# Optimization experiments

Measured on AMD Instinct MI355X. Metric: run time of the kernel, lower is better.

Reference implementation:

```python
import jax, jax.numpy as jnp
import numpy as np

EPS = 1e-5
NH, KD, D = 16, 16, 64  # num_heads, key_dim, per-head value dim (attn_ratio*key_dim)


def _bn(x, g, b):
    # train-mode BatchNorm1d over [B, C, N]: stats over (B, N), biased variance
    m = jnp.mean(x, axis=(0, 2), keepdims=True)
    v = jnp.var(x, axis=(0, 2), keepdims=True)
    return (x - m) * jax.lax.rsqrt(v + EPS) * g[None, :, None] + b[None, :, None]


def _relu6(x):
    return jnp.clip(x, 0.0, 6.0)


def setup_inputs() -> dict:
    key = jax.random.key(0)
    ks = jax.random.split(key, 8)
    B, C, H, W = 8, 256, 32, 32
    dim, dh, hid = 256, NH * D, 1024

    def w(k, shape):
        return jax.random.normal(k, shape, dtype=jnp.float32) * 0.02

    return {
        "x": jax.random.normal(ks[0], (B, C, H, W), dtype=jnp.float32),
        "g1": jnp.ones((dim,), jnp.float32), "b1": jnp.zeros((dim,), jnp.float32),
        "wq": w(ks[1], (NH * KD, dim)), "bq": jnp.zeros((NH * KD,), jnp.float32),
        "wk": w(ks[2], (NH * KD, dim)), "bk": jnp.zeros((NH * KD,), jnp.float32),
        "wv": w(ks[3], (dh, dim)), "bv": jnp.zeros((dh,), jnp.float32),
        "wp": w(ks[4], (dim, dh)), "bp": jnp.zeros((dim,), jnp.float32),
        "g2": jnp.ones((dim,), jnp.float32), "b2": jnp.zeros((dim,), jnp.float32),
        "w1": w(ks[5], (hid, dim)), "bb1": jnp.zeros((hid,), jnp.float32),
        "w2": w(ks[6], (dim, hid)), "bb2": jnp.zeros((dim,), jnp.float32),
    }


def reference(x, g1, b1, wq, bq, wk, bk, wv, bv, wp, bp, g2, b2, w1, bb1, w2, bb2):
    B, C, H, W = x.shape
    N = H * W
    xf = x.reshape(B, C, N)

    # --- attention branch (dropout is identity in eval/reference) ---
    y = _bn(xf, g1, b1)
    q = (jnp.einsum('bcn,oc->bon', y, wq) + bq[None, :, None]).reshape(B, NH, KD, N).transpose(0, 1, 3, 2)  # [B,h,N,kd]
    k = jnp.einsum('bcn,oc->bon', y, wk) + bk[None, :, None]
    k = k.reshape(B, NH, KD, N)                                                                           # [B,h,kd,N]
    v = (jnp.einsum('bcn,oc->bon', y, wv) + bv[None, :, None]).reshape(B, NH, D, N).transpose(0, 1, 3, 2)  # [B,h,N,d]
    # torch code divides by scale = key_dim**-0.5, i.e. multiplies by sqrt(key_dim)
    attn = jax.nn.softmax(jnp.einsum('bhnk,bhkm->bhnm', q, k) / (KD ** -0.5), axis=-1)
    o = jnp.einsum('bhnm,bhmd->bhnd', attn, v).transpose(0, 1, 3, 2).reshape(B, NH * D, N)                 # [B,dh,N]
    o = jnp.einsum('bdn,od->bon', o, wp) + bp[None, :, None]                                               # [B,C,N]
    xf = xf + o

    # --- MLP branch: Linear(dim->hid) + ReLU6 + Conv1d(hid->dim, k=1) ---
    y2 = _bn(xf, g2, b2)
    h = _relu6(jnp.einsum('bcn,hc->bhn', y2, w1) + bb1[None, :, None])
    m = jnp.einsum('bhn,oh->bon', h, w2) + bb2[None, :, None]
    xf = xf + m

    return xf.reshape(B, C, H, W)
```

## Files before the change

### kernel.cpp

```cpp
#include <hip/hip_runtime.h>
#include <hip/hip_bf16.h>
#include <cstdint>


typedef __attribute__((ext_vector_type(8))) short short8;
typedef __attribute__((ext_vector_type(4))) float floatx4;

#define QK_SC 5.770780163555851f

__device__ __forceinline__ float b2f(unsigned short u) {
  union { unsigned int i; float f; } x; x.i = ((unsigned int)u) << 16; return x.f;
}
__device__ __forceinline__ unsigned short f2b(float f) {
  union { float f; unsigned int i; } x; x.f = f;
  unsigned int r = x.i + 0x7FFFu + ((x.i >> 16) & 1u);
  return (unsigned short)(r >> 16);
}
__device__ __forceinline__ unsigned int f2b2(float a, float b) {
  __hip_bfloat162 h = __float22bfloat162_rn(make_float2(a, b));
  union { __hip_bfloat162 v; unsigned int u; } x; x.v = h; return x.u;
}

__global__ __launch_bounds__(256) void prep(
    const float* __restrict__ s0, const float* __restrict__ s1,
    const float* __restrict__ s2, const float* __restrict__ s3,
    const float* __restrict__ s4, const float* __restrict__ s5,
    unsigned short* __restrict__ dst,
    const float* __restrict__ x, float* __restrict__ acc,
    const float* __restrict__ bq, const float* __restrict__ bk,
    const float* __restrict__ bv, float* __restrict__ biasqkv) {
  int blk = blockIdx.x, t = threadIdx.x;
  if (blk < 1152) {
    int i = blk * 256 + t;
    if (i >= 294912) return;
    const float* s; int li; size_t dbase;
    if (i < 16384)       { s = s0; li = i;          dbase = 0; }
    else if (i < 32768)  { s = s1; li = i - 16384;  dbase = 65536; }
    else if (i < 98304)  { s = s2; li = i - 32768;  dbase = 131072; }
    else if (i < 163840) { s = s3; li = i - 98304;  dbase = 393216; }
    else if (i < 229376) { s = s4; li = i - 163840; dbase = 655360; }
    else                 { s = s5; li = i - 229376; dbase = 917504; }
    float4 v = ((const float4*)s)[li];
    uint2 o; o.x = f2b2(v.x, v.y); o.y = f2b2(v.z, v.w);
    ((uint2*)(dst + dbase))[li] = o;
  } else if (blk < 3200) {
    int blk2 = blk - 1152;
    int b = blk2 >> 8, c = blk2 & 255;
    const float* p = x + (((size_t)(b * 256 + c)) << 10);
    float4 v = ((const float4*)p)[t];
    float s = (v.x + v.y) + (v.z + v.w);
    float s2 = (v.x * v.x + v.y * v.y) + (v.z * v.z + v.w * v.w);
    #pragma unroll
    for (int o = 32; o > 0; o >>= 1) { s += __shfl_down(s, o, 64); s2 += __shfl_down(s2, o, 64); }
    __shared__ float rs[4], rs2[4];
    int w = t >> 6;
    if ((t & 63) == 0) { rs[w] = s; rs2[w] = s2; }
    __syncthreads();
    if (t == 0) {
      atomicAdd(acc + c, (rs[0] + rs[1]) + (rs[2] + rs[3]));
      atomicAdd(acc + 256 + c, (rs2[0] + rs2[1]) + (rs2[2] + rs2[3]));
    }
  } else {
    int i = (blk - 3200) * 256 + t;
    float v = (i < 256) ? bq[i] : (i < 512) ? bk[i - 256] : bv[i - 512];
    biasqkv[i] = v;
  }
}

__global__ __launch_bounds__(256) void bn_apply_t(
    const float* __restrict__ x, const float* __restrict__ acc,
    const float* __restrict__ g, const float* __restrict__ bb,
    unsigned short* __restrict__ yt) {
  int nt = blockIdx.x, ct = blockIdx.y, b = blockIdx.z;
  int t = threadIdx.x;
  __shared__ unsigned short T[64][72];
  {
    int r = t >> 2, g4 = (t & 3) * 16;
    int c = ct * 64 + r;
    float m = acc[c] * (1.0f / 8192.0f);
    float var = acc[256 + c] * (1.0f / 8192.0f) - m * m;
    float scl = g[c] * rsqrtf(var + 1e-5f);
    float shf = bb[c] - m * scl;
    const float* p = x + (((size_t)(b * 256 + c)) << 10) + nt * 64 + g4;
    float4 u0 = *(const float4*)(p);
    float4 u1 = *(const float4*)(p + 4);
    float4 u2 = *(const float4*)(p + 8);
    float4 u3 = *(const float4*)(p + 12);
    uint4 o0, o1;
    o0.x = f2b2(fmaf(u0.x, scl, shf), fmaf(u0.y, scl, shf));
    o0.y = f2b2(fmaf(u0.z, scl, shf), fmaf(u0.w, scl, shf));
    o0.z = f2b2(fmaf(u1.x, scl, shf), fmaf(u1.y, scl, shf));
    o0.w = f2b2(fmaf(u1.z, scl, shf), fmaf(u1.w, scl, shf));
    o1.x = f2b2(fmaf(u2.x, scl, shf), fmaf(u2.y, scl, shf));
    o1.y = f2b2(fmaf(u2.z, scl, shf), fmaf(u2.w, scl, shf));
    o1.z = f2b2(fmaf(u3.x, scl, shf), fmaf(u3.y, scl, shf));
    o1.w = f2b2(fmaf(u3.z, scl, shf), fmaf(u3.w, scl, shf));
    *(uint4*)&T[r][g4] = o0;
    *(uint4*)&T[r][g4 + 8] = o1;
  }
  __syncthreads();
  {
    int nr = t >> 2, cg = (t & 3) * 16;
    unsigned int ob[8];
    #pragma unroll
    for (int j = 0; j < 8; ++j) {
      unsigned int lo = T[cg + 2 * j][nr];
      unsigned int hi = T[cg + 2 * j + 1][nr];
      ob[j] = lo | (hi << 16);
    }
    unsigned short* orow = yt + ((size_t)(b * 1024 + nt * 64 + nr)) * 256 + ct * 64 + cg;
    *(uint4*)&orow[0] = make_uint4(ob[0], ob[1], ob[2], ob[3]);
    *(uint4*)&orow[8] = make_uint4(ob[4], ob[5], ob[6], ob[7]);
  }
}

template <int MODE>
__global__ __launch_bounds__(256, 4) void gemm3(
    const unsigned short* __restrict__ W, const unsigned short* __restrict__ Bn,
    const float* __restrict__ bias, const float* __restrict__ resf,
    const unsigned short* __restrict__ resb, void* __restrict__ outv,
    float* __restrict__ stats, const float* __restrict__ bnin,
    const float* __restrict__ g, const float* __restrict__ bb, int M, int K) {
  int bid = blockIdx.x;
  int b = bid & 7;
  int rest = bid >> 3;
  int n0 = (rest & 15) * 64, m0 = (rest >> 4) * 64;
  int t = threadIdx.x, lane = t & 63, w = t >> 6;
  int ml = lane & 15, quad = lane >> 4;

  __shared__ unsigned short Wt[64][72];
  __shared__ unsigned short Yt[64][72];
  __shared__ float Scl[256], Shf[256];

  if (MODE == 6) {
    float m = bnin[t] * (1.0f / 8192.0f);
    float var = bnin[256 + t] * (1.0f / 8192.0f) - m * m;
    float scl = g[t] * rsqrtf(var + 1e-5f);
    Scl[t] = scl;
    Shf[t] = bb[t] - m * scl;
    __syncthreads();
  }

  const unsigned short* Bp = Bn + (size_t)b * 1024 * K;
  int sr = t >> 2, scg = (t & 3) * 16;
  const unsigned short* wrow = W + (size_t)(m0 + sr) * K + scg;
  const unsigned short* brow = Bp + (size_t)(n0 + sr) * K + scg;

  floatx4 acc[4];
  #pragma unroll
  for (int i = 0; i < 4; ++i) acc[i] = (floatx4){0.f, 0.f, 0.f, 0.f};

  for (int k0 = 0; k0 < K; k0 += 64) {
    *(uint4*)&Wt[sr][scg]     = *(const uint4*)(wrow + k0);
    *(uint4*)&Wt[sr][scg + 8] = *(const uint4*)(wrow + k0 + 8);
    if (MODE == 6) {
      uint4 r0 = *(const uint4*)(brow + k0);
      uint4 r1 = *(const uint4*)(brow + k0 + 8);
      int cb = k0 + scg;
      float4 s0 = *(const float4*)&Scl[cb],     h0 = *(const float4*)&Shf[cb];
      float4 s1 = *(const float4*)&Scl[cb + 4], h1 = *(const float4*)&Shf[cb + 4];
      float4 s2 = *(const float4*)&Scl[cb + 8], h2 = *(const float4*)&Shf[cb + 8];
      float4 s3 = *(const float4*)&Scl[cb + 12], h3 = *(const float4*)&Shf[cb + 12];
      uint4 o0, o1;
      o0.x = f2b2(fmaf(b2f(r0.x & 0xffff), s0.x, h0.x), fmaf(b2f(r0.x >> 16), s0.y, h0.y));
      o0.y = f2b2(fmaf(b2f(r0.y & 0xffff), s0.z, h0.z), fmaf(b2f(r0.y >> 16), s0.w, h0.w));
      o0.z = f2b2(fmaf(b2f(r0.z & 0xffff), s1.x, h1.x), fmaf(b2f(r0.z >> 16), s1.y, h1.y));
      o0.w = f2b2(fmaf(b2f(r0.w & 0xffff), s1.z, h1.z), fmaf(b2f(r0.w >> 16), s1.w, h1.w));
      o1.x = f2b2(fmaf(b2f(r1.x & 0xffff), s2.x, h2.x), fmaf(b2f(r1.x >> 16), s2.y, h2.y));
      o1.y = f2b2(fmaf(b2f(r1.y & 0xffff), s2.z, h2.z), fmaf(b2f(r1.y >> 16), s2.w, h2.w));
      o1.z = f2b2(fmaf(b2f(r1.z & 0xffff), s3.x, h3.x), fmaf(b2f(r1.z >> 16), s3.y, h3.y));
      o1.w = f2b2(fmaf(b2f(r1.w & 0xffff), s3.z, h3.z), fmaf(b2f(r1.w >> 16), s3.w, h3.w));
      *(uint4*)&Yt[sr][scg]     = o0;
      *(uint4*)&Yt[sr][scg + 8] = o1;
    } else {
      *(uint4*)&Yt[sr][scg]     = *(const uint4*)(brow + k0);
      *(uint4*)&Yt[sr][scg + 8] = *(const uint4*)(brow + k0 + 8);
    }
    __syncthreads();
    short8 a0 = *(const short8*)&Wt[w * 16 + ml][quad * 8];
    short8 a1 = *(const short8*)&Wt[w * 16 + ml][32 + quad * 8];
    #pragma unroll
    for (int nt2 = 0; nt2 < 4; ++nt2) {
      short8 b0 = *(const short8*)&Yt[nt2 * 16 + ml][quad * 8];
      short8 b1 = *(const short8*)&Yt[nt2 * 16 + ml][32 + quad * 8];
      acc[nt2] = __builtin_amdgcn_mfma_f32_16x16x32_bf16(a0, b0, acc[nt2], 0, 0, 0);
      acc[nt2] = __builtin_amdgcn_mfma_f32_16x16x32_bf16(a1, b1, acc[nt2], 0, 0, 0);
    }
    __syncthreads();
  }

  int row_base = m0 + w * 16 + quad * 4;

  if (MODE == 4) {
    int hh = row_base >> 4;
    float b0 = bias[row_base + 0], b1 = bias[row_base + 1];
    float b2 = bias[row_base + 2], b3 = bias[row_base + 3];
    if (hh < 32) {
      unsigned short* qkout = (unsigned short*)outv + ((hh < 16) ? 0 : 2097152);
      float os = (hh < 16) ? QK_SC : 1.0f;
      int head = hh & 15, kd0 = row_base & 15;
      #pragma unroll
      for (int c = 0; c < 4; ++c) {
        int col = n0 + c * 16 + ml;
        uint2 pw;
        pw.x = f2b2((acc[c][0] + b0) * os, (acc[c][1] + b1) * os);
        pw.y = f2b2((acc[c][2] + b2) * os, (acc[c][3] + b3) * os);
        *(uint2*)&qkout[(((size_t)b * 16 + head) * 1024 + col) * 16 + kd0] = pw;
      }
    } else {
      unsigned short* vout = (unsigned short*)outv + 4194304;
      int d0 = row_base - 512;
      #pragma unroll
      for (int c = 0; c < 4; ++c) {
        int col = n0 + c * 16 + ml;
        vout[((size_t)b * 1024 + d0 + 0) * 1024 + col] = f2b(acc[c][0] + b0);
        vout[((size_t)b * 1024 + d0 + 1) * 1024 + col] = f2b(acc[c][1] + b1);
        vout[((size_t)b * 1024 + d0 + 2) * 1024 + col] = f2b(acc[c][2] + b2);
        vout[((size_t)b * 1024 + d0 + 3) * 1024 + col] = f2b(acc[c][3] + b3);
      }
    }
  } else if (MODE == 5) {
    unsigned short* outp = (unsigned short*)outv;
    float vsum[4] = {0.f, 0.f, 0.f, 0.f}, vsq[4] = {0.f, 0.f, 0.f, 0.f};
    #pragma unroll
    for (int c = 0; c < 4; ++c) {
      int col = n0 + c * 16 + ml;
      float v0 = acc[c][0] + bias[row_base + 0] + resf[((size_t)b * 256 + row_base + 0) * 1024 + col];
      float v1 = acc[c][1] + bias[row_base + 1] + resf[((size_t)b * 256 + row_base + 1) * 1024 + col];
      float v2 = acc[c][2] + bias[row_base + 2] + resf[((size_t)b * 256 + row_base + 2) * 1024 + col];
      float v3 = acc[c][3] + bias[row_base + 3] + resf[((size_t)b * 256 + row_base + 3) * 1024 + col];
      vsum[0] += v0; vsq[0] += v0 * v0;
      vsum[1] += v1; vsq[1] += v1 * v1;
      vsum[2] += v2; vsq[2] += v2 * v2;
      vsum[3] += v3; vsq[3] += v3 * v3;
      uint2 pw; pw.x = f2b2(v0, v1); pw.y = f2b2(v2, v3);
      *(uint2*)&outp[((size_t)b * 1024 + col) * 256 + row_base] = pw;
    }
    #pragma unroll
    for (int r = 0; r < 4; ++r) {
      float s = vsum[r], q = vsq[r];
      #pragma unroll
      for (int o = 1; o < 16; o <<= 1) { s += __shfl_xor(s, o, 64); q += __shfl_xor(q, o, 64); }
      if (ml == 0) {
        atomicAdd(stats + row_base + r, s);
        atomicAdd(stats + 256 + row_base + r, q);
      }
    }
  } else if (MODE == 6) {
    unsigned short* outp = (unsigned short*)outv;
    #pragma unroll
    for (int c = 0; c < 4; ++c) {
      int col = n0 + c * 16 + ml;
      float v0 = fminf(fmaxf(acc[c][0] + bias[row_base + 0], 0.f), 6.f);
      float v1 = fminf(fmaxf(acc[c][1] + bias[row_base + 1], 0.f), 6.f);
      float v2 = fminf(fmaxf(acc[c][2] + bias[row_base + 2], 0.f), 6.f);
      float v3 = fminf(fmaxf(acc[c][3] + bias[row_base + 3], 0.f), 6.f);
      uint2 pw; pw.x = f2b2(v0, v1); pw.y = f2b2(v2, v3);
      *(uint2*)&outp[((size_t)b * 1024 + col) * 1024 + row_base] = pw;
    }
  } else {
    float* outp = (float*)outv;
    #pragma unroll
    for (int c = 0; c < 4; ++c) {
      int col = n0 + c * 16 + ml;
      uint2 rv = *(const uint2*)(resb + ((size_t)b * 1024 + col) * 256 + row_base);
      float r0 = b2f((unsigned short)(rv.x & 0xffff));
      float r1 = b2f((unsigned short)(rv.x >> 16));
      float r2 = b2f((unsigned short)(rv.y & 0xffff));
      float r3 = b2f((unsigned short)(rv.y >> 16));
      outp[((size_t)b * 256 + row_base + 0) * 1024 + col] = acc[c][0] + bias[row_base + 0] + r0;
      outp[((size_t)b * 256 + row_base + 1) * 1024 + col] = acc[c][1] + bias[row_base + 1] + r1;
      outp[((size_t)b * 256 + row_base + 2) * 1024 + col] = acc[c][2] + bias[row_base + 2] + r2;
      outp[((size_t)b * 256 + row_base + 3) * 1024 + col] = acc[c][3] + bias[row_base + 3] + r3;
    }
  }
}

__global__ __launch_bounds__(256, 4) void attn_kernel(
    const unsigned short* __restrict__ qt, const unsigned short* __restrict__ kt,
    const unsigned short* __restrict__ vt, unsigned short* __restrict__ ot) {
  int bx0 = blockIdx.x;
  int bx = (bx0 & 7) * 128 + (bx0 >> 3);
  int nt = bx & 7, h = (bx >> 3) & 15, b = bx >> 7;
  int tid = threadIdx.x, lane = tid & 63, w = tid >> 6;
  int ml = lane & 15, quad = lane >> 4;

  __shared__ unsigned int Pscr[4][2][2][16][18];
  __shared__ float Ssum[4][2][16];

  const int n0 = nt * 128 + w * 32;
  const size_t qk_row = ((size_t)b * 16 + h) * 1024;

  short8 qf[2];
  #pragma unroll
  for (int rg = 0; rg < 2; ++rg) {
    short8 z = {0, 0, 0, 0, 0, 0, 0, 0};
    if (quad < 2)
      z = *(const short8*)(qt + (qk_row + n0 + rg * 16 + ml) * 16 + quad * 8);
    qf[rg] = z;
  }

  const floatx4 zf = {0.f, 0.f, 0.f, 0.f};
  floatx4 oacc[2][4];
  #pragma unroll
  for (int rg = 0; rg < 2; ++rg)
    #pragma unroll
    for (int dt = 0; dt < 4; ++dt) oacc[rg][dt] = zf;
  float psum0 = 0.f, psum1 = 0.f;

  const unsigned short* kp = kt + qk_row * 16;
  const unsigned short* vp = vt + ((size_t)b * 1024 + h * 64) * 1024;

  #pragma unroll 2
  for (int mc = 0; mc < 1024; mc += 32) {
    int buf = (mc >> 5) & 1;
    short8 kf[2];
    #pragma unroll
    for (int tt = 0; tt < 2; ++tt) {
      short8 z = {0, 0, 0, 0, 0, 0, 0, 0};
      if (quad < 2)
        z = *(const short8*)(kp + (size_t)(mc + tt * 16 + ml) * 16 + quad * 8);
      kf[tt] = z;
    }
    short8 vf[4];
    #pragma unroll
    for (int dt = 0; dt < 4; ++dt)
      vf[dt] = *(const short8*)(vp + (size_t)(dt * 16 + ml) * 1024 + mc + quad * 8);

    #pragma unroll
    for (int rg = 0; rg < 2; ++rg) {
      #pragma unroll
      for (int tt = 0; tt < 2; ++tt) {
        floatx4 s = __builtin_amdgcn_mfma_f32_16x16x32_bf16(kf[tt], qf[rg], zf, 0, 0, 0);
        float p0 = __builtin_amdgcn_exp2f(s[0]);
        float p1 = __builtin_amdgcn_exp2f(s[1]);
        float p2 = __builtin_amdgcn_exp2f(s[2]);
        float p3 = __builtin_amdgcn_exp2f(s[3]);
        if (rg == 0) psum0 += (p0 + p1) + (p2 + p3);
        else         psum1 += (p0 + p1) + (p2 + p3);
        uint2 pw; pw.x = f2b2(p0, p1); pw.y = f2b2(p2, p3);
        *(uint2*)&Pscr[w][buf][rg][ml][tt * 8 + quad * 2] = pw;
      }
    }
    #pragma unroll
    for (int rg = 0; rg < 2; ++rg) {
      uint2 a0 = *(const uint2*)&Pscr[w][buf][rg][ml][quad * 4];
      uint2 a1 = *(const uint2*)&Pscr[w][buf][rg][ml][quad * 4 + 2];
      union { uint4 u; short8 s; } cv;
      cv.u = make_uint4(a0.x, a0.y, a1.x, a1.y);
      short8 af = cv.s;
      #pragma unroll
      for (int dt = 0; dt < 4; ++dt)
        oacc[rg][dt] = __builtin_amdgcn_mfma_f32_16x16x32_bf16(af, vf[dt], oacc[rg][dt], 0, 0, 0);
    }
  }

  {
    float s0 = psum0;
    s0 += __shfl_xor(s0, 16, 64);
    s0 += __shfl_xor(s0, 32, 64);
    float s1 = psum1;
    s1 += __shfl_xor(s1, 16, 64);
    s1 += __shfl_xor(s1, 32, 64);
    if (lane < 16) { Ssum[w][0][ml] = s0; Ssum[w][1][ml] = s1; }
  }
  #pragma unroll
  for (int rg = 0; rg < 2; ++rg) {
    float4 sv = *(const float4*)&Ssum[w][rg][quad * 4];
    float inv0 = 1.0f / sv.x, inv1 = 1.0f / sv.y;
    float inv2 = 1.0f / sv.z, inv3 = 1.0f / sv.w;
    int nbase = n0 + rg * 16 + quad * 4;
    #pragma unroll
    for (int dt = 0; dt < 4; ++dt) {
      int dg = h * 64 + dt * 16 + ml;
      size_t obase = (((size_t)b << 10) + nbase) * 1024 + dg;
      ot[obase + 0 * 1024] = f2b(oacc[rg][dt][0] * inv0);
      ot[obase + 1 * 1024] = f2b(oacc[rg][dt][1] * inv1);
      ot[obase + 2 * 1024] = f2b(oacc[rg][dt][2] * inv2);
      ot[obase + 3 * 1024] = f2b(oacc[rg][dt][3] * inv3);
    }
  }
}

extern "C" void kernel_launch(void* const* d_in, const int* in_sizes, int n_in,
                              void* d_out, int out_size, void* d_ws, size_t ws_size,
                              hipStream_t stream) {
  const float* x   = (const float*)d_in[0];
  const float* g1  = (const float*)d_in[1];
  const float* b1  = (const float*)d_in[2];
  const float* wq  = (const float*)d_in[3];
  const float* bq  = (const float*)d_in[4];
  const float* wk  = (const float*)d_in[5];
  const float* bk  = (const float*)d_in[6];
  const float* wv  = (const float*)d_in[7];
  const float* bv  = (const float*)d_in[8];
  const float* wp  = (const float*)d_in[9];
  const float* bp  = (const float*)d_in[10];
  const float* g2  = (const float*)d_in[11];
  const float* b2  = (const float*)d_in[12];
  const float* w1  = (const float*)d_in[13];
  const float* bb1 = (const float*)d_in[14];
  const float* w2  = (const float*)d_in[15];
  const float* bb2 = (const float*)d_in[16];

  char* ws = (char*)d_ws;
  float* bnacc   = (float*)ws;
  float* biasqkv = (float*)(ws + 4096);
  unsigned short* y_t  = (unsigned short*)(ws + 16384);
  unsigned short* qt   = y_t + (size_t)2 * 1024 * 1024;
  unsigned short* kt   = qt  + (size_t)2 * 1024 * 1024;
  unsigned short* vt   = kt  + (size_t)2 * 1024 * 1024;
  unsigned short* ot   = vt  + (size_t)8 * 1024 * 1024;
  unsigned short* xf1t = ot  + (size_t)8 * 1024 * 1024;
  unsigned short* wb   = xf1t + (size_t)2 * 1024 * 1024;
  unsigned short* hb_t = ot;
  float* outp = (float*)d_out;

  unsigned short* wqkvb = wb;
  unsigned short* wpb = wb + 393216;
  unsigned short* w1b = wb + 655360;
  unsigned short* w2b = wb + 917504;
  const unsigned short* nub = nullptr;
  const float* nuf = nullptr;

  hipMemsetAsync(bnacc, 0, 4096, stream);
  prep<<<dim3(3206), dim3(256), 0, stream>>>(
      wq, wk, wv, wp, w1, w2, wb, x, bnacc, bq, bk, bv, biasqkv);

  bn_apply_t<<<dim3(16, 4, 8), dim3(256), 0, stream>>>(x, bnacc, g1, b1, y_t);
  gemm3<4><<<dim3(3072), dim3(256), 0, stream>>>(
      wqkvb, y_t, biasqkv, nuf, nub, qt, nullptr, nuf, nuf, nuf, 1536, 256);
  attn_kernel<<<dim3(1024), dim3(256), 0, stream>>>(qt, kt, vt, ot);
  gemm3<5><<<dim3(512), dim3(256), 0, stream>>>(
      wpb, ot, bp, x, nub, xf1t, bnacc + 512, nuf, nuf, nuf, 256, 1024);

  gemm3<6><<<dim3(2048), dim3(256), 0, stream>>>(
      w1b, xf1t, bb1, nuf, nub, hb_t, nullptr, bnacc + 512, g2, b2, 1024, 256);
  gemm3<7><<<dim3(512), dim3(256), 0, stream>>>(
      w2b, hb_t, bb2, nuf, xf1t, outp, nullptr, nuf, nuf, nuf, 256, 1024);
}
```

Baseline: 245.0 us.

## Software-pipeline attention loop: prefetch next K/V tiles and overlap QK with PV

Restructures the attention inner loop into a two-stage software pipeline. K and V for upcoming tiles are loaded into double-buffered registers, and the QK^T/exp step for the next tile is interleaved with the PV MFMA for the previous tile. The goal is to hide global-load latency and the LDS round-trip of P behind matrix work. In exchange it raises register pressure, which could reduce occupancy.

```diff
diff --git a/kernel.cpp b/kernel.cpp
--- a/kernel.cpp
+++ b/kernel.cpp
@@ -311,22 +311,23 @@
   const unsigned short* kp = kt + qk_row * 16;
   const unsigned short* vp = vt + ((size_t)b * 1024 + h * 64) * 1024;
 
-  #pragma unroll 2
-  for (int mc = 0; mc < 1024; mc += 32) {
-    int buf = (mc >> 5) & 1;
-    short8 kf[2];
+  auto loadK = [&](int tile, short8* dst) {
+    int mc = tile << 5;
     #pragma unroll
     for (int tt = 0; tt < 2; ++tt) {
       short8 z = {0, 0, 0, 0, 0, 0, 0, 0};
       if (quad < 2)
         z = *(const short8*)(kp + (size_t)(mc + tt * 16 + ml) * 16 + quad * 8);
-      kf[tt] = z;
-    }
-    short8 vf[4];
+      dst[tt] = z;
+    }
+  };
+  auto loadV = [&](int tile, short8* dst) {
+    int mc = tile << 5;
     #pragma unroll
     for (int dt = 0; dt < 4; ++dt)
-      vf[dt] = *(const short8*)(vp + (size_t)(dt * 16 + ml) * 1024 + mc + quad * 8);
-
+      dst[dt] = *(const short8*)(vp + (size_t)(dt * 16 + ml) * 1024 + mc + quad * 8);
+  };
+  auto qkstep = [&](const short8* kf, int bufidx) {
     #pragma unroll
     for (int rg = 0; rg < 2; ++rg) {
       #pragma unroll
@@ -339,20 +340,56 @@
         if (rg == 0) psum0 += (p0 + p1) + (p2 + p3);
         else         psum1 += (p0 + p1) + (p2 + p3);
         uint2 pw; pw.x = f2b2(p0, p1); pw.y = f2b2(p2, p3);
-        *(uint2*)&Pscr[w][buf][rg][ml][tt * 8 + quad * 2] = pw;
+        *(uint2*)&Pscr[w][bufidx][rg][ml][tt * 8 + quad * 2] = pw;
       }
     }
+  };
+  auto readP = [&](int bufidx, short8* af) {
     #pragma unroll
     for (int rg = 0; rg < 2; ++rg) {
-      uint2 a0 = *(const uint2*)&Pscr[w][buf][rg][ml][quad * 4];
-      uint2 a1 = *(const uint2*)&Pscr[w][buf][rg][ml][quad * 4 + 2];
+      uint2 a0 = *(const uint2*)&Pscr[w][bufidx][rg][ml][quad * 4];
+      uint2 a1 = *(const uint2*)&Pscr[w][bufidx][rg][ml][quad * 4 + 2];
       union { uint4 u; short8 s; } cv;
       cv.u = make_uint4(a0.x, a0.y, a1.x, a1.y);
-      short8 af = cv.s;
+      af[rg] = cv.s;
+    }
+  };
+  auto pvstep = [&](const short8* af, const short8* vf) {
+    #pragma unroll
+    for (int rg = 0; rg < 2; ++rg)
       #pragma unroll
       for (int dt = 0; dt < 4; ++dt)
-        oacc[rg][dt] = __builtin_amdgcn_mfma_f32_16x16x32_bf16(af, vf[dt], oacc[rg][dt], 0, 0, 0);
-    }
+        oacc[rg][dt] = __builtin_amdgcn_mfma_f32_16x16x32_bf16(af[rg], vf[dt], oacc[rg][dt], 0, 0, 0);
+  };
+
+  short8 kfA[2], kfB[2], vfA[4], vfB[4];
+
+  loadK(0, kfA); loadV(0, vfA);
+  qkstep(kfA, 0);
+  loadK(1, kfB); loadV(1, vfB);
+
+  for (int j = 0; j < 15; ++j) {
+    int i = 2 * j + 1;
+    short8 pa[2];
+    readP(0, pa);
+    loadK(i + 1, kfA);
+    qkstep(kfB, 1);
+    pvstep(pa, vfA);
+    loadV(i + 1, vfA);
+    readP(1, pa);
+    loadK(i + 2, kfB);
+    qkstep(kfA, 0);
+    pvstep(pa, vfB);
+    loadV(i + 2, vfB);
+  }
+
+  {
+    short8 pa[2];
+    readP(0, pa);
+    qkstep(kfB, 1);
+    pvstep(pa, vfA);
+    readP(1, pa);
+    pvstep(pa, vfB);
   }
 
   {
```

New measurement: 268.2 us. +9.5%, slower.

## Split attention key range across two wave groups with LDS reduction

Applied to the files above, without the earlier changes.

Doubles the attention block to 512 threads. Each of the two 4-wave halves processes half of the 1024 keys for the same 128 queries, and the partial outputs and row sums are combined through shared memory before normalization. The softmax has no max subtraction, so the two partials can simply be added. This halves the serial loop length per wave and raises wave-level parallelism, at the cost of extra LDS traffic, two block barriers and higher per-block register/LDS pressure.

```diff
diff --git a/kernel.cpp b/kernel.cpp
--- a/kernel.cpp
+++ b/kernel.cpp
@@ -276,19 +276,20 @@
   }
 }
 
-__global__ __launch_bounds__(256, 4) void attn_kernel(
+__global__ __launch_bounds__(512, 8) void attn_kernel(
     const unsigned short* __restrict__ qt, const unsigned short* __restrict__ kt,
     const unsigned short* __restrict__ vt, unsigned short* __restrict__ ot) {
   int bx0 = blockIdx.x;
   int bx = (bx0 & 7) * 128 + (bx0 >> 3);
   int nt = bx & 7, h = (bx >> 3) & 15, b = bx >> 7;
   int tid = threadIdx.x, lane = tid & 63, w = tid >> 6;
+  int wq_ = w & 3, half = w >> 2;
   int ml = lane & 15, quad = lane >> 4;
 
-  __shared__ unsigned int Pscr[4][2][2][16][18];
-  __shared__ float Ssum[4][2][16];
-
-  const int n0 = nt * 128 + w * 32;
+  __shared__ unsigned int Pscr[8][2][2][16][18];
+  __shared__ float Ssum[8][2][16];
+
+  const int n0 = nt * 128 + wq_ * 32;
   const size_t qk_row = ((size_t)b * 16 + h) * 1024;
 
   short8 qf[2];
@@ -311,8 +312,9 @@
   const unsigned short* kp = kt + qk_row * 16;
   const unsigned short* vp = vt + ((size_t)b * 1024 + h * 64) * 1024;
 
+  const int mbeg = half * 512, mend = mbeg + 512;
   #pragma unroll 2
-  for (int mc = 0; mc < 1024; mc += 32) {
+  for (int mc = mbeg; mc < mend; mc += 32) {
     int buf = (mc >> 5) & 1;
     short8 kf[2];
     #pragma unroll
@@ -364,20 +366,46 @@
     s1 += __shfl_xor(s1, 32, 64);
     if (lane < 16) { Ssum[w][0][ml] = s0; Ssum[w][1][ml] = s1; }
   }
-  #pragma unroll
-  for (int rg = 0; rg < 2; ++rg) {
-    float4 sv = *(const float4*)&Ssum[w][rg][quad * 4];
-    float inv0 = 1.0f / sv.x, inv1 = 1.0f / sv.y;
-    float inv2 = 1.0f / sv.z, inv3 = 1.0f / sv.w;
-    int nbase = n0 + rg * 16 + quad * 4;
-    #pragma unroll
-    for (int dt = 0; dt < 4; ++dt) {
-      int dg = h * 64 + dt * 16 + ml;
-      size_t obase = (((size_t)b << 10) + nbase) * 1024 + dg;
-      ot[obase + 0 * 1024] = f2b(oacc[rg][dt][0] * inv0);
-      ot[obase + 1 * 1024] = f2b(oacc[rg][dt][1] * inv1);
-      ot[obase + 2 * 1024] = f2b(oacc[rg][dt][2] * inv2);
-      ot[obase + 3 * 1024] = f2b(oacc[rg][dt][3] * inv3);
+
+  __syncthreads();
+  float* scr = (float*)&Pscr[0][0][0][0][0];
+  if (w >= 4) {
+    int base = ((w - 4) * 64 + lane) * 32;
+    #pragma unroll
+    for (int rg = 0; rg < 2; ++rg)
+      #pragma unroll
+      for (int dt = 0; dt < 4; ++dt) {
+        int g = rg * 4 + dt;
+        *(floatx4*)&scr[base + ((g ^ (lane & 7)) << 2)] = oacc[rg][dt];
+      }
+  }
+  __syncthreads();
+  if (w < 4) {
+    int base = (w * 64 + lane) * 32;
+    #pragma unroll
+    for (int rg = 0; rg < 2; ++rg)
+      #pragma unroll
+      for (int dt = 0; dt < 4; ++dt) {
+        int g = rg * 4 + dt;
+        floatx4 o2 = *(const floatx4*)&scr[base + ((g ^ (lane & 7)) << 2)];
+        oacc[rg][dt] += o2;
+      }
+    #pragma unroll
+    for (int rg = 0; rg < 2; ++rg) {
+      float4 svA = *(const float4*)&Ssum[w][rg][quad * 4];
+      float4 svB = *(const float4*)&Ssum[w + 4][rg][quad * 4];
+      float inv0 = 1.0f / (svA.x + svB.x), inv1 = 1.0f / (svA.y + svB.y);
+      float inv2 = 1.0f / (svA.z + svB.z), inv3 = 1.0f / (svA.w + svB.w);
+      int nbase = n0 + rg * 16 + quad * 4;
+      #pragma unroll
+      for (int dt = 0; dt < 4; ++dt) {
+        int dg = h * 64 + dt * 16 + ml;
+        size_t obase = (((size_t)b << 10) + nbase) * 1024 + dg;
+        ot[obase + 0 * 1024] = f2b(oacc[rg][dt][0] * inv0);
+        ot[obase + 1 * 1024] = f2b(oacc[rg][dt][1] * inv1);
+        ot[obase + 2 * 1024] = f2b(oacc[rg][dt][2] * inv2);
+        ot[obase + 3 * 1024] = f2b(oacc[rg][dt][3] * inv3);
+      }
     }
   }
 }
@@ -430,7 +458,7 @@
   bn_apply_t<<<dim3(16, 4, 8), dim3(256), 0, stream>>>(x, bnacc, g1, b1, y_t);
   gemm3<4><<<dim3(3072), dim3(256), 0, stream>>>(
       wqkvb, y_t, biasqkv, nuf, nub, qt, nullptr, nuf, nuf, nuf, 1536, 256);
-  attn_kernel<<<dim3(1024), dim3(256), 0, stream>>>(qt, kt, vt, ot);
+  attn_kernel<<<dim3(1024), dim3(512), 0, stream>>>(qt, kt, vt, ot);
   gemm3<5><<<dim3(512), dim3(256), 0, stream>>>(
       wpb, ot, bp, x, nub, xf1t, bnacc + 512, nuf, nuf, nuf, 256, 1024);
 
```

Result: slower. 519.9 us (+112.2%).

## Load GEMM tiles directly into LDS with XOR-swizzled layout

Applied to the files above, without the earlier changes.

Replaces the register-staged global-to-LDS tile copies in gemm3 with global_load_lds direct transfers. The padded LDS tiles become unpadded 64x64 tiles with an XOR swizzle on 16-byte column groups, so direct loads and MFMA operand reads avoid bank conflicts. The BN-fused MODE 6 path still stages through registers but writes with the same swizzle. This aims to cut VGPR traffic and LDS write instructions, but the single-buffered loop still synchronises after every step.

```diff
diff --git a/kernel.cpp b/kernel.cpp
--- a/kernel.cpp
+++ b/kernel.cpp
@@ -19,6 +19,11 @@
 __device__ __forceinline__ unsigned int f2b2(float a, float b) {
   __hip_bfloat162 h = __float22bfloat162_rn(make_float2(a, b));
   union { __hip_bfloat162 v; unsigned int u; } x; x.v = h; return x.u;
+}
+__device__ __forceinline__ void gload16(const unsigned short* g, unsigned short* l) {
+  __builtin_amdgcn_global_load_lds(
+      (const __attribute__((address_space(1))) unsigned int*)g,
+      (__attribute__((address_space(3))) unsigned int*)l, 16, 0, 0);
 }
 
 __global__ __launch_bounds__(256) void prep(
@@ -128,8 +133,8 @@
   int t = threadIdx.x, lane = t & 63, w = t >> 6;
   int ml = lane & 15, quad = lane >> 4;
 
-  __shared__ unsigned short Wt[64][72];
-  __shared__ unsigned short Yt[64][72];
+  __shared__ unsigned short Wt[64][64];
+  __shared__ unsigned short Yt[64][64];
   __shared__ float Scl[256], Shf[256];
 
   if (MODE == 6) {
@@ -143,16 +148,25 @@
 
   const unsigned short* Bp = Bn + (size_t)b * 1024 * K;
   int sr = t >> 2, scg = (t & 3) * 16;
-  const unsigned short* wrow = W + (size_t)(m0 + sr) * K + scg;
   const unsigned short* brow = Bp + (size_t)(n0 + sr) * K + scg;
+
+  int lrow = lane >> 3;
+  int cgs  = (lane & 7) ^ lrow;
+
+  char* Wb = (char*)&Wt[0][0];
+  char* Yb = (char*)&Yt[0][0];
+  const int swa = (ml & 7) << 4;
 
   floatx4 acc[4];
   #pragma unroll
   for (int i = 0; i < 4; ++i) acc[i] = (floatx4){0.f, 0.f, 0.f, 0.f};
 
   for (int k0 = 0; k0 < K; k0 += 64) {
-    *(uint4*)&Wt[sr][scg]     = *(const uint4*)(wrow + k0);
-    *(uint4*)&Wt[sr][scg + 8] = *(const uint4*)(wrow + k0 + 8);
+    #pragma unroll
+    for (int j = 0; j < 2; ++j) {
+      int row = w * 16 + j * 8 + lrow;
+      gload16(W + (size_t)(m0 + row) * K + k0 + cgs * 8, &Wt[w * 16 + j * 8][0]);
+    }
     if (MODE == 6) {
       uint4 r0 = *(const uint4*)(brow + k0);
       uint4 r1 = *(const uint4*)(brow + k0 + 8);
@@ -170,19 +184,25 @@
       o1.y = f2b2(fmaf(b2f(r1.y & 0xffff), s2.z, h2.z), fmaf(b2f(r1.y >> 16), s2.w, h2.w));
       o1.z = f2b2(fmaf(b2f(r1.z & 0xffff), s3.x, h3.x), fmaf(b2f(r1.z >> 16), s3.y, h3.y));
       o1.w = f2b2(fmaf(b2f(r1.w & 0xffff), s3.z, h3.z), fmaf(b2f(r1.w >> 16), s3.w, h3.w));
-      *(uint4*)&Yt[sr][scg]     = o0;
-      *(uint4*)&Yt[sr][scg + 8] = o1;
+      int sg0 = (t & 3) * 2, sg1 = sg0 + 1;
+      *(uint4*)(Yb + sr * 128 + ((sg0 ^ (sr & 7)) << 4)) = o0;
+      *(uint4*)(Yb + sr * 128 + ((sg1 ^ (sr & 7)) << 4)) = o1;
     } else {
-      *(uint4*)&Yt[sr][scg]     = *(const uint4*)(brow + k0);
-      *(uint4*)&Yt[sr][scg + 8] = *(const uint4*)(brow + k0 + 8);
+      #pragma unroll
+      for (int j = 0; j < 2; ++j) {
+        int row = w * 16 + j * 8 + lrow;
+        gload16(Bp + (size_t)(n0 + row) * K + k0 + cgs * 8, &Yt[w * 16 + j * 8][0]);
+      }
     }
     __syncthreads();
-    short8 a0 = *(const short8*)&Wt[w * 16 + ml][quad * 8];
-    short8 a1 = *(const short8*)&Wt[w * 16 + ml][32 + quad * 8];
+    int arow = w * 16 + ml;
+    short8 a0 = *(const short8*)(Wb + arow * 128 + ((quad << 4) ^ swa));
+    short8 a1 = *(const short8*)(Wb + arow * 128 + (((quad + 4) << 4) ^ swa));
     #pragma unroll
     for (int nt2 = 0; nt2 < 4; ++nt2) {
-      short8 b0 = *(const short8*)&Yt[nt2 * 16 + ml][quad * 8];
-      short8 b1 = *(const short8*)&Yt[nt2 * 16 + ml][32 + quad * 8];
+      int brw = nt2 * 16 + ml;
+      short8 b0 = *(const short8*)(Yb + brw * 128 + ((quad << 4) ^ swa));
+      short8 b1 = *(const short8*)(Yb + brw * 128 + (((quad + 4) << 4) ^ swa));
       acc[nt2] = __builtin_amdgcn_mfma_f32_16x16x32_bf16(a0, b0, acc[nt2], 0, 0, 0);
       acc[nt2] = __builtin_amdgcn_mfma_f32_16x16x32_bf16(a1, b1, acc[nt2], 0, 0, 0);
     }
```

After: 239.9 us. -2.1%, faster.
